# Optimization experiments

Measured on AMD Instinct MI355X. Metric: run time of the kernel, lower is better.

Reference implementation:

```python
import jax, jax.numpy as jnp
import numpy as np

NLOC = 10  # local nodes per element (cubic DG triangle)


def setup_inputs() -> dict:
    key = jax.random.key(0)
    ks = jax.random.split(key, 6)
    nele, nloc, ngi = 500000, NLOC, 13
    return {
        "r0": jax.random.normal(ks[0], (nele * nloc,), dtype=jnp.float32),
        "c_i": jax.random.normal(ks[1], (nele * nloc,), dtype=jnp.float32),
        "c_n": jax.random.normal(ks[2], (nele, 1, nloc), dtype=jnp.float32),
        "k": jnp.ones((1,), dtype=jnp.float32),
        "dt": jnp.ones((1,), dtype=jnp.float32),
        "n": jax.random.normal(ks[3], (nloc, ngi), dtype=jnp.float32),
        "nx": jax.random.normal(ks[4], (nele, 2, nloc, ngi), dtype=jnp.float32),
        "detwei": jax.random.uniform(ks[5], (nele, ngi), dtype=jnp.float32),
    }


def reference(r0, c_i, c_n, k, dt, n, nx, detwei):
    nele, _, nloc, ngi = nx.shape
    c_i = c_i.reshape(nele, 1, nloc)               # [e,1,l]
    # stiffness: sum over spatial dims of grad-grad quadrature contraction
    nx1nx1 = jnp.einsum('eig,ejg,eg->eij', nx[:, 0], nx[:, 0], detwei)
    nx2nx2 = jnp.einsum('eig,ejg,eg->eij', nx[:, 1], nx[:, 1], detwei)
    nxnx = (nx1nx1 + nx2nx2) * k                   # [e,i,j] * [1]
    # mass matrix per element (shared shape funcs, per-element detwei)
    nn = jnp.einsum('ig,jg,eg->eij', n, n, detwei)
    # transient branch (config.isTransient = True)
    nn_dt = nn / dt
    nxnx = nn_dt + nxnx
    r0 = r0.reshape(nele, nloc, 1)
    r0 = r0 + jnp.matmul(nn_dt, jnp.swapaxes(c_n, 1, 2))   # [e,i,1]
    r0 = r0.reshape(-1)
    r0 = r0 - jnp.matmul(nxnx, jnp.swapaxes(c_i, 1, 2)).reshape(-1)
    diagA = jnp.diagonal(nxnx, axis1=-2, axis2=-1)          # [e,nloc]
    bdiagA = nxnx
    return (bdiagA, diagA, r0)
```

## Files before the change

### kernel.cpp

```cpp
#include <hip/hip_runtime.h>

#define NLOC  10
#define NGI   13
#define NPAIR 55
#define EPB   64
#define TPB   256

#define BUF_FL   17472
#define W_N      (2 * BUF_FL)
#define W_TOT    (W_N + 130)

#define NX_GRAN  4160
#define TOT_GRAN 4368

typedef float vf2 __attribute__((ext_vector_type(2)));

__device__ __forceinline__ constexpr int pidx(int i, int j) {
    return i * NLOC - (i * (i - 1)) / 2 + (j - i);
}

__device__ __forceinline__ void stage16(const float* gsrc, float* lds) {
    __builtin_amdgcn_global_load_lds(
        (const __attribute__((address_space(1))) void*)gsrc,
        (__attribute__((address_space(3))) void*)lds, 16, 0, 0);
}

__global__ __launch_bounds__(TPB) void fem_kernel(
    const float* __restrict__ r0g,
    const float* __restrict__ cig,
    const float* __restrict__ cng,
    const float* __restrict__ kp,
    const float* __restrict__ dtp,
    const float* __restrict__ nmat,
    const float* __restrict__ nx,
    const float* __restrict__ dwei,
    float* __restrict__ out,
    int nele)
{
    __shared__ float sm[W_TOT];

    const int t       = threadIdx.x;
    const int nchunks = (nele + EPB - 1) / EPB;
    const int gs      = gridDim.x;

    if (t < 130) sm[W_N + t] = nmat[t];

    auto stage_chunk = [&](int b, int c) {
        const long ce0   = (long)c * EPB;
        const int  crem  = min(EPB, nele - (int)ce0);
        const int  capnx = crem * 260;
        const int  capdw = crem * 13;
        const float* nxsrc = nx   + (size_t)ce0 * 260;
        const float* dwsrc = dwei + (size_t)ce0 * 13;
        float* ldsb = sm + b * BUF_FL + (t >> 6) * 256;
        #pragma unroll
        for (int k = 0; k < 18; ++k) {
            const int G = k * 256 + t;
            if (G < NX_GRAN) {
                if (G * 4 < capnx) stage16(nxsrc + (size_t)G * 4, ldsb + k * 1024);
            } else if (G < TOT_GRAN) {
                const int rel = G - NX_GRAN;
                if (rel * 4 < capdw) stage16(dwsrc + (size_t)rel * 4, ldsb + k * 1024);
            }
        }
    };

    const int  eloc = t >> 2;
    const int  d    = (t >> 1) & 1;
    const int  h    = t & 1;
    const int  q    = t & 3;
    const float kk  = kp[0];
    const float idt = 1.0f / dtp[0];
    const float* smn = sm + W_N;

    int c = blockIdx.x;
    if (c < nchunks) stage_chunk(0, c);
    __syncthreads();

    int cur = 0;
    for (; c < nchunks; c += gs) {
        const int next = c + gs;
        if (next < nchunks) stage_chunk(cur ^ 1, next);
        const long e0   = (long)c * EPB;
        const int  rem  = min(EPB, nele - (int)e0);
        const long e    = e0 + eloc;
        const bool live = eloc < rem;
        const long ee   = live ? e : (long)(nele - 1);

        const float* smnx = sm + cur * BUF_FL + eloc * 260 + d * 130;
        const float* smdw = sm + cur * BUF_FL + 16640 + eloc * 13;

        float civ[NLOC], dif[NLOC];
        {
            const vf2* ci2 = reinterpret_cast<const vf2*>(cig + (size_t)ee * 10);
            const vf2* cn2 = reinterpret_cast<const vf2*>(cng + (size_t)ee * 10);
            #pragma unroll
            for (int u2 = 0; u2 < 5; ++u2) {
                vf2 a = ci2[u2], b = cn2[u2];
                civ[2*u2]   = a.x; civ[2*u2+1] = a.y;
                dif[2*u2]   = b.x - a.x; dif[2*u2+1] = b.y - a.y;
            }
        }

        float acc[NPAIR];
        #pragma unroll
        for (int p = 0; p < NPAIR; ++p) acc[p] = 0.0f;
        float r0a[NLOC];
        #pragma unroll
        for (int i = 0; i < NLOC; ++i) r0a[i] = 0.0f;

        #pragma unroll
        for (int it = 0; it < 7; ++it) {
            const int   graw = 2 * it + h;
            const int   g    = graw < NGI ? graw : NGI - 1;
            const float wv   = graw < NGI ? kk * smdw[g] : 0.0f;
            float col[NLOC];
            #pragma unroll
            for (int l = 0; l < NLOC; ++l) col[l] = smnx[l * 13 + g];
            float u = 0.0f;
            #pragma unroll
            for (int l = 0; l < NLOC; ++l) u = fmaf(col[l], civ[l], u);
            const float uw = u * wv;
            #pragma unroll
            for (int i = 0; i < NLOC; ++i) {
                const float ti = col[i] * wv;
                #pragma unroll
                for (int j = i; j < NLOC; ++j)
                    acc[pidx(i, j)] = fmaf(ti, col[j], acc[pidx(i, j)]);
                r0a[i] = fmaf(-col[i], uw, r0a[i]);
            }
        }

        #pragma unroll
        for (int it = 0; it < 4; ++it) {
            const int   graw = q + 4 * it;
            const int   g    = graw < NGI ? graw : NGI - 1;
            const float wv   = graw < NGI ? idt * smdw[g] : 0.0f;
            float ncol[NLOC];
            #pragma unroll
            for (int l = 0; l < NLOC; ++l) ncol[l] = smn[l * 13 + g];
            float wd = 0.0f;
            #pragma unroll
            for (int l = 0; l < NLOC; ++l) wd = fmaf(ncol[l], dif[l], wd);
            #pragma unroll
            for (int i = 0; i < NLOC; ++i) {
                const float ti = ncol[i] * wv;
                #pragma unroll
                for (int j = i; j < NLOC; ++j)
                    acc[pidx(i, j)] = fmaf(ti, ncol[j], acc[pidx(i, j)]);
                r0a[i] = fmaf(ti, wd, r0a[i]);
            }
        }

        #pragma unroll
        for (int p = 0; p < NPAIR; ++p) {
            acc[p] += __shfl_xor(acc[p], 1);
            acc[p] += __shfl_xor(acc[p], 2);
        }
        #pragma unroll
        for (int i = 0; i < NLOC; ++i) {
            r0a[i] += __shfl_xor(r0a[i], 1);
            r0a[i] += __shfl_xor(r0a[i], 2);
        }

        if (live) {
            float* obd = out + (size_t)e * 100;
            float* odg = out + (size_t)nele * 100 + (size_t)e * 10;
            float* oro = out + (size_t)nele * 110 + (size_t)e * 10;
            const float* r0s = r0g + (size_t)e * 10;
            #pragma unroll
            for (int i = 0; i < NLOC; ++i) {
                if ((i & 3) == q) {
                    float row[NLOC];
                    #pragma unroll
                    for (int j = 0; j < NLOC; ++j) {
                        const int lo = i < j ? i : j, hi = i < j ? j : i;
                        row[j] = acc[pidx(lo, hi)];
                    }
                    #pragma unroll
                    for (int u2 = 0; u2 < 5; ++u2) {
                        vf2 v = { row[2*u2], row[2*u2+1] };
                        *reinterpret_cast<vf2*>(obd + i * 10 + 2 * u2) = v;
                    }
                    odg[i] = row[i];
                    oro[i] = r0s[i] + r0a[i];
                }
            }
        }

        __syncthreads();
        cur ^= 1;
    }
}

extern "C" void kernel_launch(void* const* d_in, const int* in_sizes, int n_in,
                              void* d_out, int out_size, void* d_ws, size_t ws_size,
                              hipStream_t stream) {
    const float* r0   = (const float*)d_in[0];
    const float* ci   = (const float*)d_in[1];
    const float* cn   = (const float*)d_in[2];
    const float* k    = (const float*)d_in[3];
    const float* dt   = (const float*)d_in[4];
    const float* nmat = (const float*)d_in[5];
    const float* nx   = (const float*)d_in[6];
    const float* dw   = (const float*)d_in[7];
    const int nele = in_sizes[7] / NGI;

    const int nchunks = (nele + EPB - 1) / EPB;
    const int nb = min(256, nchunks);
    fem_kernel<<<nb, TPB, 0, stream>>>(r0, ci, cn, k, dt, nmat, nx, dw,
                                       (float*)d_out, nele);
}
```

Before: 249.2 us.

## Stage r0, c_i, c_n through async LDS double buffer with smaller blocks

Extends the asynchronous global-to-LDS staging so that r0, c_i and c_n are prefetched into the double buffer alongside nx and detwei, instead of being read directly from global memory during compute. The block is halved to 32 elements and 128 threads, the grid is doubled to 512 blocks, and launch bounds now request one block per SM hint. The aim is to hide the latency of the per-element vector loads behind the compute of the previous chunk. In exchange, each block stages less data per iteration, and the new block and grid sizes change occupancy.

```diff
diff --git a/kernel.cpp b/kernel.cpp
--- a/kernel.cpp
+++ b/kernel.cpp
@@ -3,15 +3,23 @@
 #define NLOC  10
 #define NGI   13
 #define NPAIR 55
-#define EPB   64
-#define TPB   256
-
-#define BUF_FL   17472
-#define W_N      (2 * BUF_FL)
-#define W_TOT    (W_N + 130)
-
-#define NX_GRAN  4160
-#define TOT_GRAN 4368
+#define EPB   32
+#define TPB   128
+
+#define B_NX   0
+#define B_DW   8320
+#define B_R0   8736
+#define B_CI   9056
+#define B_CN   9376
+#define BUF_FL 9696
+#define W_N    (2 * BUF_FL)
+#define W_TOT  (W_N + 130)
+
+#define GE_NX  2080
+#define GE_DW  2184
+#define GE_R0  2264
+#define GE_CI  2344
+#define GE_CN  2424
 
 typedef float vf2 __attribute__((ext_vector_type(2)));
 
@@ -25,7 +33,7 @@
         (__attribute__((address_space(3))) void*)lds, 16, 0, 0);
 }
 
-__global__ __launch_bounds__(TPB) void fem_kernel(
+__global__ __launch_bounds__(TPB, 1) void fem_kernel(
     const float* __restrict__ r0g,
     const float* __restrict__ cig,
     const float* __restrict__ cng,
@@ -43,25 +51,27 @@
     const int nchunks = (nele + EPB - 1) / EPB;
     const int gs      = gridDim.x;
 
-    if (t < 130) sm[W_N + t] = nmat[t];
-
     auto stage_chunk = [&](int b, int c) {
-        const long ce0   = (long)c * EPB;
-        const int  crem  = min(EPB, nele - (int)ce0);
-        const int  capnx = crem * 260;
-        const int  capdw = crem * 13;
-        const float* nxsrc = nx   + (size_t)ce0 * 260;
-        const float* dwsrc = dwei + (size_t)ce0 * 13;
+        const long ce0  = (long)c * EPB;
+        const int  crem = min(EPB, nele - (int)ce0);
+        const float* snx = nx   + (size_t)ce0 * 260;
+        const float* sdw = dwei + (size_t)ce0 * 13;
+        const float* sr0 = r0g  + (size_t)ce0 * 10;
+        const float* sci = cig  + (size_t)ce0 * 10;
+        const float* scn = cng  + (size_t)ce0 * 10;
+        const int cnx = crem * 260, cdw = crem * 13, c10 = crem * 10;
         float* ldsb = sm + b * BUF_FL + (t >> 6) * 256;
         #pragma unroll
-        for (int k = 0; k < 18; ++k) {
-            const int G = k * 256 + t;
-            if (G < NX_GRAN) {
-                if (G * 4 < capnx) stage16(nxsrc + (size_t)G * 4, ldsb + k * 1024);
-            } else if (G < TOT_GRAN) {
-                const int rel = G - NX_GRAN;
-                if (rel * 4 < capdw) stage16(dwsrc + (size_t)rel * 4, ldsb + k * 1024);
-            }
+        for (int k = 0; k < 19; ++k) {
+            const int G = k * TPB + t;
+            const float* src; int rel, capf;
+            if      (G < GE_NX) { src = snx; rel = G;         capf = cnx; }
+            else if (G < GE_DW) { src = sdw; rel = G - GE_NX; capf = cdw; }
+            else if (G < GE_R0) { src = sr0; rel = G - GE_DW; capf = c10; }
+            else if (G < GE_CI) { src = sci; rel = G - GE_R0; capf = c10; }
+            else if (G < GE_CN) { src = scn; rel = G - GE_CI; capf = c10; }
+            else continue;
+            if (rel * 4 < capf) stage16(src + (size_t)rel * 4, ldsb + k * TPB * 4);
         }
     };
 
@@ -75,32 +85,31 @@
 
     int c = blockIdx.x;
     if (c < nchunks) stage_chunk(0, c);
+    for (int w = t; w < 130; w += TPB) sm[W_N + w] = nmat[w];
     __syncthreads();
 
     int cur = 0;
     for (; c < nchunks; c += gs) {
         const int next = c + gs;
         if (next < nchunks) stage_chunk(cur ^ 1, next);
+
         const long e0   = (long)c * EPB;
         const int  rem  = min(EPB, nele - (int)e0);
         const long e    = e0 + eloc;
         const bool live = eloc < rem;
-        const long ee   = live ? e : (long)(nele - 1);
-
-        const float* smnx = sm + cur * BUF_FL + eloc * 260 + d * 130;
-        const float* smdw = sm + cur * BUF_FL + 16640 + eloc * 13;
+
+        const float* bb   = sm + cur * BUF_FL;
+        const float* smnx = bb + B_NX + eloc * 260 + d * 130;
+        const float* smdw = bb + B_DW + eloc * 13;
+        const float* smr0 = bb + B_R0 + eloc * 10;
+        const float* smci = bb + B_CI + eloc * 10;
+        const float* smcn = bb + B_CN + eloc * 10;
 
         float civ[NLOC], dif[NLOC];
-        {
-            const vf2* ci2 = reinterpret_cast<const vf2*>(cig + (size_t)ee * 10);
-            const vf2* cn2 = reinterpret_cast<const vf2*>(cng + (size_t)ee * 10);
-            #pragma unroll
-            for (int u2 = 0; u2 < 5; ++u2) {
-                vf2 a = ci2[u2], b = cn2[u2];
-                civ[2*u2]   = a.x; civ[2*u2+1] = a.y;
-                dif[2*u2]   = b.x - a.x; dif[2*u2+1] = b.y - a.y;
-            }
-        }
+        #pragma unroll
+        for (int l = 0; l < NLOC; ++l) civ[l] = smci[l];
+        #pragma unroll
+        for (int l = 0; l < NLOC; ++l) dif[l] = smcn[l] - civ[l];
 
         float acc[NPAIR];
         #pragma unroll
@@ -167,7 +176,6 @@
             float* obd = out + (size_t)e * 100;
             float* odg = out + (size_t)nele * 100 + (size_t)e * 10;
             float* oro = out + (size_t)nele * 110 + (size_t)e * 10;
-            const float* r0s = r0g + (size_t)e * 10;
             #pragma unroll
             for (int i = 0; i < NLOC; ++i) {
                 if ((i & 3) == q) {
@@ -183,7 +191,7 @@
                         *reinterpret_cast<vf2*>(obd + i * 10 + 2 * u2) = v;
                     }
                     odg[i] = row[i];
-                    oro[i] = r0s[i] + r0a[i];
+                    oro[i] = smr0[i] + r0a[i];
                 }
             }
         }
@@ -207,7 +215,7 @@
     const int nele = in_sizes[7] / NGI;
 
     const int nchunks = (nele + EPB - 1) / EPB;
-    const int nb = min(256, nchunks);
+    const int nb = min(512, nchunks);
     fem_kernel<<<nb, TPB, 0, stream>>>(r0, ci, cn, k, dt, nmat, nx, dw,
                                        (float*)d_out, nele);
 }
```

Result: faster. 210.7 us (-15.5%).
